# Performance work log

Hardware: AMD Instinct MI355X
Metric: run time of the kernel (lower is better)

The kernel has to match this reference:

```python
import jax, jax.numpy as jnp
import numpy as np

N_NODES = 100000
N_EDGES = 1600000
N_FEAT = 256
HIDDEN = 128


def setup_inputs() -> dict:
    key = jax.random.key(0)
    k1, k2, k3, k4 = jax.random.split(key, 4)
    x = jax.random.normal(k1, (N_NODES, N_FEAT), dtype=jnp.float32)
    edge_index = jax.random.randint(k2, (2, N_EDGES), 0, N_NODES, dtype=jnp.int64)
    # GCNConv linear weight (PyG Linear: out = x @ W.T), bias added after aggregation
    W = jax.random.normal(k3, (HIDDEN, N_FEAT), dtype=jnp.float32) / np.sqrt(N_FEAT)
    b = jnp.zeros((HIDDEN,), dtype=jnp.float32)
    # PReLU per-channel slope, torch default init 0.25
    prelu_a = jnp.full((HIDDEN,), 0.25, dtype=jnp.float32)
    return {"x": x, "edge_index": edge_index, "W": W, "b": b, "prelu_a": prelu_a}


def reference(x, edge_index, W, b, prelu_a):
    N = x.shape[0]
    # dense linear transform first (as PyG GCNConv does)
    h = x @ W.T  # [N, hidden]
    # add self-loops
    loops = jnp.arange(N, dtype=edge_index.dtype)
    row = jnp.concatenate([edge_index[0], loops])  # source
    col = jnp.concatenate([edge_index[1], loops])  # target
    # symmetric normalization: deg computed over target index (PyG gcn_norm)
    ones = jnp.ones(row.shape[0], dtype=h.dtype)
    deg = jax.ops.segment_sum(ones, col, num_segments=N)
    dinv = jnp.where(deg > 0, jax.lax.rsqrt(deg), 0.0)
    norm = dinv[row] * dinv[col]  # [E+N]
    # gather source features, scale, scatter-sum to targets
    msg = h[row] * norm[:, None]  # [E+N, hidden]
    agg = jax.ops.segment_sum(msg, col, num_segments=N) + b  # [N, hidden]
    # PReLU with per-channel slope
    return jnp.where(agg > 0, agg, prelu_a * agg)
```

## Files before the change

### kernel.cpp

```cpp
#include <hip/hip_runtime.h>
#include <hip/hip_fp16.h>
#include <stdint.h>

#define N_NODES 100000
#define N_EDGES 1600000
#define N_FEAT 256
#define HIDDEN 128
#define SCAN_CHUNK 1024
#define NB ((N_NODES + SCAN_CHUNK - 1) / SCAN_CHUNK)

#define BKT_SH 8
#define BKT_RANGE 256
#define NBKT ((N_NODES + BKT_RANGE - 1) >> BKT_SH)
#define BKT_CAP 4608
#define BIN_CHUNK 4096
#define NWG_BIN ((N_EDGES + BIN_CHUNK - 1) / BIN_CHUNK)

typedef __attribute__((ext_vector_type(8))) _Float16 f16x8;
typedef __attribute__((ext_vector_type(4))) float f32x4;


__global__ __launch_bounds__(256) void k_wconv_zero(const float* __restrict__ W,
                                                    short* __restrict__ w16,
                                                    int* __restrict__ gcur) {
    int i = blockIdx.x * 256 + threadIdx.x;
    if (i < HIDDEN * N_FEAT) {
        __half h = __float2half_rn(W[i]);
        w16[i] = *(short*)&h;
    }
    if (i < NBKT) gcur[i] = 0;
}


__global__ __launch_bounds__(256) void k_bin(const int* __restrict__ row,
                                             const int* __restrict__ col,
                                             int* __restrict__ gcur,
                                             int2* __restrict__ recs) {
    __shared__ int hcnt[NBKT];
    __shared__ int hbase[NBKT];
    const int t = threadIdx.x;
    for (int i = t; i < NBKT; i += 256) hcnt[i] = 0;
    __syncthreads();
    const int e0 = blockIdx.x * BIN_CHUNK;
    int cs[16], ss[16];
#pragma unroll
    for (int i = 0; i < 16; ++i) {
        int e = e0 + t + i * 256;
        if (e < N_EDGES) {
            cs[i] = col[e];
            ss[i] = row[e];
            atomicAdd(&hcnt[cs[i] >> BKT_SH], 1);
        } else {
            cs[i] = -1;
        }
    }
    __syncthreads();
    for (int i = t; i < NBKT; i += 256) {
        int c = hcnt[i];
        hbase[i] = (c > 0) ? atomicAdd(&gcur[i], c) : 0;
    }
    __syncthreads();
    for (int i = t; i < NBKT; i += 256) hcnt[i] = 0;
    __syncthreads();
#pragma unroll
    for (int i = 0; i < 16; ++i) {
        if (cs[i] >= 0) {
            int bkt = cs[i] >> BKT_SH;
            int pos = hbase[bkt] + atomicAdd(&hcnt[bkt], 1);
            if (pos < BKT_CAP)
                recs[(size_t)bkt * BKT_CAP + pos] = make_int2(cs[i], ss[i]);
        }
    }
}


__global__ __launch_bounds__(256) void k_hist(const int* __restrict__ gcur,
                                              const int2* __restrict__ recs,
                                              int* __restrict__ cnt,
                                              float* __restrict__ dinv) {
    __shared__ int hc[BKT_RANGE];
    const int b = blockIdx.x, t = threadIdx.x;
    hc[t] = 0;
    __syncthreads();
    int n = gcur[b];
    if (n > BKT_CAP) n = BKT_CAP;
    const int2* rb = recs + (size_t)b * BKT_CAP;
    for (int i = t; i < n; i += 256)
        atomicAdd(&hc[rb[i].x & (BKT_RANGE - 1)], 1);
    __syncthreads();
    int node = (b << BKT_SH) + t;
    if (node < N_NODES) {
        cnt[node] = hc[t];
        dinv[node] = rsqrtf((float)(hc[t] + 1));
    }
}


__global__ __launch_bounds__(256) void k_scan1(const int* __restrict__ cnt,
                                               int* __restrict__ row_ptr,
                                               int* __restrict__ bsum) {
    __shared__ int ts[256];
    int t = threadIdx.x;
    int base = blockIdx.x * SCAN_CHUNK + t * 4;
    int v[4];
#pragma unroll
    for (int i = 0; i < 4; ++i) { int idx = base + i; v[i] = (idx < N_NODES) ? cnt[idx] : 0; }
    int s = v[0] + v[1] + v[2] + v[3];
    int val = s;
    ts[t] = val;
    __syncthreads();
    for (int off = 1; off < 256; off <<= 1) {
        int other = (t >= off) ? ts[t - off] : 0;
        __syncthreads();
        val += other;
        ts[t] = val;
        __syncthreads();
    }
    int run = val - s;
#pragma unroll
    for (int i = 0; i < 4; ++i) {
        int idx = base + i;
        if (idx < N_NODES) row_ptr[idx] = run;
        run += v[i];
    }
    if (t == 255) bsum[blockIdx.x] = val;
}

__global__ void k_scan2(int* __restrict__ bsum, int* __restrict__ row_ptr) {
    if (threadIdx.x == 0) {
        int run = 0;
        for (int i = 0; i < NB; ++i) { int v = bsum[i]; bsum[i] = run; run += v; }
        row_ptr[N_NODES] = run;
    }
}

__global__ __launch_bounds__(256) void k_scan3(int* __restrict__ row_ptr,
                                               const int* __restrict__ bsum) {
    int t = threadIdx.x;
    int base = blockIdx.x * SCAN_CHUNK + t * 4;
    int add = bsum[blockIdx.x];
#pragma unroll
    for (int i = 0; i < 4; ++i) {
        int idx = base + i;
        if (idx < N_NODES) row_ptr[idx] += add;
    }
}


__global__ __launch_bounds__(256) void k_slot2(const int* __restrict__ gcur,
                                               const int2* __restrict__ recs,
                                               const int* __restrict__ row_ptr,
                                               int* __restrict__ edge_src) {
    __shared__ int cur[BKT_RANGE];
    __shared__ int rp[BKT_RANGE];
    const int b = blockIdx.x, t = threadIdx.x;
    cur[t] = 0;
    int node = (b << BKT_SH) + t;
    rp[t] = (node < N_NODES) ? row_ptr[node] : 0;
    __syncthreads();
    int n = gcur[b];
    if (n > BKT_CAP) n = BKT_CAP;
    const int2* rb = recs + (size_t)b * BKT_CAP;
    for (int i = t; i < n; i += 256) {
        int2 r = rb[i];
        int l = r.x & (BKT_RANGE - 1);
        int pos = rp[l] + atomicAdd(&cur[l], 1);
        edge_src[pos] = r.y;
    }
}

#define TM 64
#define KS 32
#define LDR 40

__global__ __launch_bounds__(256) void k_gemm(const float* __restrict__ x,
                                              const short* __restrict__ w16,
                                              const float* __restrict__ dinv,
                                              __half* __restrict__ h2) {
    __shared__ short xh[TM * LDR];
    __shared__ short wh[HIDDEN * LDR];
    const int t = threadIdx.x;
    const int lane = t & 63;
    const int wv = t >> 6;
    const int wr = wv >> 1, wc = wv & 1;
    const int row0 = blockIdx.x * TM;

    f32x4 acc[2][4];
#pragma unroll
    for (int m = 0; m < 2; ++m)
#pragma unroll
        for (int n = 0; n < 4; ++n) acc[m][n] = (f32x4)0.f;

    const int rx = t >> 2, sx = t & 3;
    const int gxr = row0 + rx;
    const bool xok = (gxr < N_NODES);
    const int rw0 = t >> 2, rw1 = (t >> 2) + 64, slw = t & 3;

    for (int k0 = 0; k0 < N_FEAT; k0 += KS) {
        float4 f[2];
#pragma unroll
        for (int q = 0; q < 2; ++q) {
            f[q] = make_float4(0.f, 0.f, 0.f, 0.f);
            if (xok) f[q] = *(const float4*)&x[(size_t)gxr * N_FEAT + k0 + sx * 8 + q * 4];
        }
        {
            __half2 p0 = __floats2half2_rn(f[0].x, f[0].y);
            __half2 p1 = __floats2half2_rn(f[0].z, f[0].w);
            __half2 p2 = __floats2half2_rn(f[1].x, f[1].y);
            __half2 p3 = __floats2half2_rn(f[1].z, f[1].w);
            int4 pk = make_int4(*(int*)&p0, *(int*)&p1, *(int*)&p2, *(int*)&p3);
            *(int4*)&xh[rx * LDR + sx * 8] = pk;
        }
        {
            int4 a0 = *(const int4*)&w16[(size_t)rw0 * N_FEAT + k0 + slw * 8];
            int4 a1 = *(const int4*)&w16[(size_t)rw1 * N_FEAT + k0 + slw * 8];
            *(int4*)&wh[rw0 * LDR + slw * 8] = a0;
            *(int4*)&wh[rw1 * LDR + slw * 8] = a1;
        }
        __syncthreads();
        const int fr = lane & 15, fs = lane >> 4;
        f16x8 ah[2], bh[4];
#pragma unroll
        for (int m = 0; m < 2; ++m) {
            int o = (wr * 32 + m * 16 + fr) * LDR + fs * 8;
            ah[m] = *(const f16x8*)&xh[o];
        }
#pragma unroll
        for (int n = 0; n < 4; ++n) {
            int o = (wc * 64 + n * 16 + fr) * LDR + fs * 8;
            bh[n] = *(const f16x8*)&wh[o];
        }
#pragma unroll
        for (int m = 0; m < 2; ++m)
#pragma unroll
            for (int n = 0; n < 4; ++n)
                acc[m][n] = __builtin_amdgcn_mfma_f32_16x16x32_f16(ah[m], bh[n], acc[m][n], 0, 0, 0);
        __syncthreads();
    }
    const int cr = (lane >> 4) * 4, cc = lane & 15;
#pragma unroll
    for (int m = 0; m < 2; ++m) {
        int gr0 = row0 + wr * 32 + m * 16 + cr;
#pragma unroll
        for (int r = 0; r < 4; ++r) {
            int gr = gr0 + r;
            if (gr < N_NODES) {
                float d = dinv[gr];
#pragma unroll
                for (int n = 0; n < 4; ++n) {
                    int gc = wc * 64 + n * 16 + cc;
                    h2[(size_t)gr * HIDDEN + gc] = __float2half_rn(acc[m][n][r] * d);
                }
            }
        }
    }
}


__global__ __launch_bounds__(256) void k_gather(const int* __restrict__ row_ptr,
                                                const int* __restrict__ edge_src,
                                                const float* __restrict__ dinv,
                                                const __half* __restrict__ h2s,
                                                const float* __restrict__ b,
                                                const float* __restrict__ pa,
                                                float* __restrict__ out) {
    int n = (blockIdx.x * 256 + threadIdx.x) >> 6;
    int lane = threadIdx.x & 63;
    if (n >= N_NODES) return;
    int start = row_ptr[n], end = row_ptr[n + 1];
    float dn = dinv[n];
    const __half2* hp = (const __half2*)h2s;
    float2 base = __half22float2(hp[(unsigned)n * 64u + lane]);
    float2 acc = make_float2(0.f, 0.f);
    for (int e = start; e < end; e += 16) {
        int idx[16];
        float wt[16];
#pragma unroll
        for (int i = 0; i < 16; ++i) {
            int ee = e + i;
            int cl = (ee < end) ? ee : (end - 1);
            idx[i] = edge_src[cl];
            wt[i] = (ee < end) ? 1.f : 0.f;
        }
        __half2 v[16];
#pragma unroll
        for (int i = 0; i < 16; ++i) v[i] = hp[(unsigned)idx[i] * 64u + lane];
#pragma unroll
        for (int i = 0; i < 16; ++i) {
            float2 f = __half22float2(v[i]);
            acc.x += f.x * wt[i];
            acc.y += f.y * wt[i];
        }
    }
    float2 bb = *(const float2*)&b[lane * 2];
    float2 aa = *(const float2*)&pa[lane * 2];
    float2 r;
    r.x = dn * (base.x + acc.x) + bb.x;
    r.y = dn * (base.y + acc.y) + bb.y;
    r.x = r.x > 0.f ? r.x : r.x * aa.x;
    r.y = r.y > 0.f ? r.y : r.y * aa.y;
    *(float2*)&out[(size_t)n * HIDDEN + lane * 2] = r;
}


extern "C" void kernel_launch(void* const* d_in, const int* in_sizes, int n_in,
                              void* d_out, int out_size, void* d_ws, size_t ws_size,
                              hipStream_t stream) {
    const float* x  = (const float*)d_in[0];
    const int*   ei = (const int*)d_in[1];
    const float* W  = (const float*)d_in[2];
    const float* b  = (const float*)d_in[3];
    const float* pa = (const float*)d_in[4];
    float* out = (float*)d_out;

    const int* row = ei;
    const int* col = ei + N_EDGES;

    char* w = (char*)d_ws;
    __half* h2      = (__half*)w;
    int*   cnt      = (int*)(w + (size_t)(N_NODES + 1) * HIDDEN * 2);
    int*   row_ptr  = cnt + N_NODES;
    int*   bsum     = row_ptr + (N_NODES + 2);
    int*   edge_src = bsum + 128;
    float* dinv     = (float*)(edge_src + N_EDGES);
    short* w16      = (short*)(dinv + N_NODES);
    int*   gcur     = (int*)(w16 + HIDDEN * N_FEAT);
    int2*  recs     = (int2*)(((uintptr_t)(gcur + NBKT) + 15) & ~(uintptr_t)15);

    k_wconv_zero<<<(HIDDEN * N_FEAT + 255) / 256, 256, 0, stream>>>(W, w16, gcur);
    k_bin<<<NWG_BIN, 256, 0, stream>>>(row, col, gcur, recs);
    k_hist<<<NBKT, 256, 0, stream>>>(gcur, recs, cnt, dinv);
    k_scan1<<<NB, 256, 0, stream>>>(cnt, row_ptr, bsum);
    k_scan2<<<1, 64, 0, stream>>>(bsum, row_ptr);
    k_scan3<<<NB, 256, 0, stream>>>(row_ptr, bsum);
    k_slot2<<<NBKT, 256, 0, stream>>>(gcur, recs, row_ptr, edge_src);
    k_gemm<<<(N_NODES + TM - 1) / TM, 256, 0, stream>>>(x, w16, dinv, h2);
    k_gather<<<(int)(((size_t)N_NODES * 64 + 255) / 256), 256, 0, stream>>>(
        row_ptr, edge_src, dinv, h2, b, pa, out);
}
```

Measured before the change: 155.9 us.

## Replace global CSR scan with per-bucket local offsets and prescaled edge indices

Drops the three-kernel global prefix scan. Each bucket's histogram block now does a local scan and writes per-node (start,end) pairs into a padded edge array laid out at fixed BKT_CAP strides, so the global row_ptr is no longer needed. Edge source indices are stored pre-shifted by 8, giving the byte offset of a fp16 row, which removes the multiply in the gather address math. The cost is a larger, sparsely filled edge_src buffer and per-node int2 loads instead of two ints.

```diff
diff --git a/kernel.cpp b/kernel.cpp
--- a/kernel.cpp
+++ b/kernel.cpp
@@ -6,8 +6,6 @@
 #define N_EDGES 1600000
 #define N_FEAT 256
 #define HIDDEN 128
-#define SCAN_CHUNK 1024
-#define NB ((N_NODES + SCAN_CHUNK - 1) / SCAN_CHUNK)
 
 #define BKT_SH 8
 #define BKT_RANGE 256
@@ -76,9 +74,10 @@
 
 __global__ __launch_bounds__(256) void k_hist(const int* __restrict__ gcur,
                                               const int2* __restrict__ recs,
-                                              int* __restrict__ cnt,
+                                              int2* __restrict__ srow,
                                               float* __restrict__ dinv) {
     __shared__ int hc[BKT_RANGE];
+    __shared__ int ts[BKT_RANGE];
     const int b = blockIdx.x, t = threadIdx.x;
     hc[t] = 0;
     __syncthreads();
@@ -88,75 +87,36 @@
     for (int i = t; i < n; i += 256)
         atomicAdd(&hc[rb[i].x & (BKT_RANGE - 1)], 1);
     __syncthreads();
+    int cnt = hc[t];
+    int val = cnt;
+    ts[t] = val;
+    __syncthreads();
+    for (int off = 1; off < 256; off <<= 1) {
+        int other = (t >= off) ? ts[t - off] : 0;
+        __syncthreads();
+        val += other;
+        ts[t] = val;
+        __syncthreads();
+    }
     int node = (b << BKT_SH) + t;
     if (node < N_NODES) {
-        cnt[node] = hc[t];
-        dinv[node] = rsqrtf((float)(hc[t] + 1));
-    }
-}
-
-
-__global__ __launch_bounds__(256) void k_scan1(const int* __restrict__ cnt,
-                                               int* __restrict__ row_ptr,
-                                               int* __restrict__ bsum) {
-    __shared__ int ts[256];
-    int t = threadIdx.x;
-    int base = blockIdx.x * SCAN_CHUNK + t * 4;
-    int v[4];
-#pragma unroll
-    for (int i = 0; i < 4; ++i) { int idx = base + i; v[i] = (idx < N_NODES) ? cnt[idx] : 0; }
-    int s = v[0] + v[1] + v[2] + v[3];
-    int val = s;
-    ts[t] = val;
-    __syncthreads();
-    for (int off = 1; off < 256; off <<= 1) {
-        int other = (t >= off) ? ts[t - off] : 0;
-        __syncthreads();
-        val += other;
-        ts[t] = val;
-        __syncthreads();
-    }
-    int run = val - s;
-#pragma unroll
-    for (int i = 0; i < 4; ++i) {
-        int idx = base + i;
-        if (idx < N_NODES) row_ptr[idx] = run;
-        run += v[i];
-    }
-    if (t == 255) bsum[blockIdx.x] = val;
-}
-
-__global__ void k_scan2(int* __restrict__ bsum, int* __restrict__ row_ptr) {
-    if (threadIdx.x == 0) {
-        int run = 0;
-        for (int i = 0; i < NB; ++i) { int v = bsum[i]; bsum[i] = run; run += v; }
-        row_ptr[N_NODES] = run;
-    }
-}
-
-__global__ __launch_bounds__(256) void k_scan3(int* __restrict__ row_ptr,
-                                               const int* __restrict__ bsum) {
-    int t = threadIdx.x;
-    int base = blockIdx.x * SCAN_CHUNK + t * 4;
-    int add = bsum[blockIdx.x];
-#pragma unroll
-    for (int i = 0; i < 4; ++i) {
-        int idx = base + i;
-        if (idx < N_NODES) row_ptr[idx] += add;
+        int start = b * BKT_CAP + (val - cnt);
+        srow[node] = make_int2(start, start + cnt);
+        dinv[node] = rsqrtf((float)(cnt + 1));
     }
 }
 
 
 __global__ __launch_bounds__(256) void k_slot2(const int* __restrict__ gcur,
                                                const int2* __restrict__ recs,
-                                               const int* __restrict__ row_ptr,
+                                               const int2* __restrict__ srow,
                                                int* __restrict__ edge_src) {
     __shared__ int cur[BKT_RANGE];
     __shared__ int rp[BKT_RANGE];
     const int b = blockIdx.x, t = threadIdx.x;
     cur[t] = 0;
     int node = (b << BKT_SH) + t;
-    rp[t] = (node < N_NODES) ? row_ptr[node] : 0;
+    rp[t] = (node < N_NODES) ? srow[node].x : 0;
     __syncthreads();
     int n = gcur[b];
     if (n > BKT_CAP) n = BKT_CAP;
@@ -165,7 +125,7 @@
         int2 r = rb[i];
         int l = r.x & (BKT_RANGE - 1);
         int pos = rp[l] + atomicAdd(&cur[l], 1);
-        edge_src[pos] = r.y;
+        edge_src[pos] = r.y << 8;
     }
 }
 
@@ -257,7 +217,7 @@
 }
 
 
-__global__ __launch_bounds__(256) void k_gather(const int* __restrict__ row_ptr,
+__global__ __launch_bounds__(256) void k_gather(const int2* __restrict__ srow,
                                                 const int* __restrict__ edge_src,
                                                 const float* __restrict__ dinv,
                                                 const __half* __restrict__ h2s,
@@ -267,10 +227,11 @@
     int n = (blockIdx.x * 256 + threadIdx.x) >> 6;
     int lane = threadIdx.x & 63;
     if (n >= N_NODES) return;
-    int start = row_ptr[n], end = row_ptr[n + 1];
+    int2 se = srow[n];
+    int start = se.x, end = se.y;
     float dn = dinv[n];
-    const __half2* hp = (const __half2*)h2s;
-    float2 base = __half22float2(hp[(unsigned)n * 64u + lane]);
+    const char* hb = (const char*)h2s + (unsigned)(lane * 4);
+    float2 base = __half22float2(*(const __half2*)(hb + (size_t)(unsigned)n * 256u));
     float2 acc = make_float2(0.f, 0.f);
     for (int e = start; e < end; e += 16) {
         int idx[16];
@@ -278,13 +239,13 @@
 #pragma unroll
         for (int i = 0; i < 16; ++i) {
             int ee = e + i;
-            int cl = (ee < end) ? ee : (end - 1);
+            int cl = min(ee, end - 1);
             idx[i] = edge_src[cl];
             wt[i] = (ee < end) ? 1.f : 0.f;
         }
         __half2 v[16];
 #pragma unroll
-        for (int i = 0; i < 16; ++i) v[i] = hp[(unsigned)idx[i] * 64u + lane];
+        for (int i = 0; i < 16; ++i) v[i] = *(const __half2*)(hb + (unsigned)idx[i]);
 #pragma unroll
         for (int i = 0; i < 16; ++i) {
             float2 f = __half22float2(v[i]);
@@ -318,23 +279,18 @@
 
     char* w = (char*)d_ws;
     __half* h2      = (__half*)w;
-    int*   cnt      = (int*)(w + (size_t)(N_NODES + 1) * HIDDEN * 2);
-    int*   row_ptr  = cnt + N_NODES;
-    int*   bsum     = row_ptr + (N_NODES + 2);
-    int*   edge_src = bsum + 128;
-    float* dinv     = (float*)(edge_src + N_EDGES);
+    int2*  srow     = (int2*)(w + (size_t)(N_NODES + 1) * HIDDEN * 2);
+    int*   edge_src = (int*)(srow + N_NODES);
+    float* dinv     = (float*)(edge_src + (size_t)NBKT * BKT_CAP);
     short* w16      = (short*)(dinv + N_NODES);
     int*   gcur     = (int*)(w16 + HIDDEN * N_FEAT);
     int2*  recs     = (int2*)(((uintptr_t)(gcur + NBKT) + 15) & ~(uintptr_t)15);
 
     k_wconv_zero<<<(HIDDEN * N_FEAT + 255) / 256, 256, 0, stream>>>(W, w16, gcur);
     k_bin<<<NWG_BIN, 256, 0, stream>>>(row, col, gcur, recs);
-    k_hist<<<NBKT, 256, 0, stream>>>(gcur, recs, cnt, dinv);
-    k_scan1<<<NB, 256, 0, stream>>>(cnt, row_ptr, bsum);
-    k_scan2<<<1, 64, 0, stream>>>(bsum, row_ptr);
-    k_scan3<<<NB, 256, 0, stream>>>(row_ptr, bsum);
-    k_slot2<<<NBKT, 256, 0, stream>>>(gcur, recs, row_ptr, edge_src);
+    k_hist<<<NBKT, 256, 0, stream>>>(gcur, recs, srow, dinv);
+    k_slot2<<<NBKT, 256, 0, stream>>>(gcur, recs, srow, edge_src);
     k_gemm<<<(N_NODES + TM - 1) / TM, 256, 0, stream>>>(x, w16, dinv, h2);
     k_gather<<<(int)(((size_t)N_NODES * 64 + 255) / 256), 256, 0, stream>>>(
-        row_ptr, edge_src, dinv, h2, b, pa, out);
-}
+        srow, edge_src, dinv, h2, b, pa, out);
+}
```

Result: faster. 148.8 us (-4.5%).
